# Kernel optimization log

Hardware: AMD Instinct MI355X
Metric: run time of the kernel (lower is better)

Reference implementation:

```python
import jax, jax.numpy as jnp
import numpy as np

K = 20          # neighbors, hardcoded in module
SLOPE = 0.2     # LeakyReLU negative slope
EPS = 1e-5      # BatchNorm eps (eval mode, running_mean=0, running_var=1)


def _knn_idx(x, k):
    # x: (B, N, C) -> (B, N, k) indices of k nearest neighbors (includes self)
    xx = jnp.sum(x * x, axis=-1)                      # (B, N)
    inner = jnp.einsum('bnc,bmc->bnm', x, x)          # (B, N, N)
    neg_sqdist = 2.0 * inner - xx[:, :, None] - xx[:, None, :]
    _, idx = jax.lax.top_k(neg_sqdist, k)
    return idx


def _graph_feature(x, k):
    # x: (B, N, C) -> edge features (B, N, k, 2C) = [x_j - x_i, x_i]
    idx = _knn_idx(x, k)
    feat = jax.vmap(lambda xt, ix: xt[ix])(x, idx)    # (B, N, k, C)
    xc = jnp.broadcast_to(x[:, :, None, :], feat.shape)
    return jnp.concatenate([feat - xc, xc], axis=-1)


def _bn_lrelu(h, g, b):
    # eval-mode BN (mean=0, var=1) + LeakyReLU(0.2)
    h = h * (g / jnp.sqrt(1.0 + EPS)) + b
    return jnp.where(h >= 0, h, SLOPE * h)


def _edge_conv(x, W, g, b):
    # EdgeConv block: graph feature -> 1x1 conv -> BN -> LeakyReLU -> max over k
    e = _graph_feature(x, K)                          # (B, N, k, 2C)
    h = jnp.einsum('bnkc,oc->bnko', e, W)
    h = _bn_lrelu(h, g, b)
    return jnp.max(h, axis=2)                         # (B, N, O)


def reference(x, W1, g1, b1, W2, g2, b2, W3, g3, b3, W4, g4, b4, W5, g5, b5, Wemb):
    # x: (B, N, 3) point cloud
    x1 = _edge_conv(x, W1, g1, b1)    # (B, N, 64)
    x2 = _edge_conv(x1, W2, g2, b2)   # (B, N, 64)
    x3 = _edge_conv(x2, W3, g3, b3)   # (B, N, 128)
    x4 = _edge_conv(x3, W4, g4, b4)   # (B, N, 256)
    h = jnp.concatenate([x1, x2, x3, x4], axis=-1)    # (B, N, 512)
    h = jnp.einsum('bnc,oc->bno', h, W5)              # conv5 (1x1)
    h = _bn_lrelu(h, g5, b5)
    h = jnp.max(h, axis=1)                            # global max pool -> (B, 512)
    feat = h[:, None, :]                              # (B, 1, 512)
    embedding = h @ Wemb.T                            # (B, 256)
    return (feat, embedding)


def setup_inputs() -> dict:
    key = jax.random.key(0)
    ks = jax.random.split(key, 18)
    B, N = 8, 2048
    num_features = 256

    def w(k, o, i):
        return jax.random.normal(k, (o, i), dtype=jnp.float32) * (1.0 / np.sqrt(i))

    return {
        'x':  jax.random.normal(ks[0], (B, N, 3), dtype=jnp.float32),
        'W1': w(ks[1], 64, 6),
        'g1': jnp.ones((64,), jnp.float32),  'b1': jnp.zeros((64,), jnp.float32),
        'W2': w(ks[2], 64, 128),
        'g2': jnp.ones((64,), jnp.float32),  'b2': jnp.zeros((64,), jnp.float32),
        'W3': w(ks[3], 128, 128),
        'g3': jnp.ones((128,), jnp.float32), 'b3': jnp.zeros((128,), jnp.float32),
        'W4': w(ks[4], 256, 256),
        'g4': jnp.ones((256,), jnp.float32), 'b4': jnp.zeros((256,), jnp.float32),
        'W5': w(ks[5], 512, 512),
        'g5': jnp.ones((512,), jnp.float32), 'b5': jnp.zeros((512,), jnp.float32),
        'Wemb': w(ks[6], num_features, 512),
    }
```

## Files before the change

kernel.cpp:

```cpp
#include <hip/hip_runtime.h>
#include <hip/hip_bf16.h>

#define BB 8
#define NN 2048
#define KK 20
#define BN (BB*NN)
#define RSQ 0.99999500003749969f

constexpr size_t OFF_XX  = 0;
constexpr size_t OFF_X1  = OFF_XX  + BN;
constexpr size_t OFF_X2  = OFF_X1  + (size_t)BN*64;
constexpr size_t OFF_X3  = OFF_X2  + (size_t)BN*64;
constexpr size_t OFF_X4  = OFF_X3  + (size_t)BN*128;
constexpr size_t OFF_SC  = OFF_X4  + (size_t)BN*256;
constexpr size_t OFF_ID  = OFF_SC  + (size_t)BN*160;
constexpr size_t OFF_W5T = OFF_ID  + (size_t)BN*20;
constexpr size_t OFF_MX  = OFF_W5T + 512*512;
constexpr size_t OFF_MN  = OFF_MX  + BB*512;
constexpr size_t OFF_WT2 = OFF_MN  + BB*512;
constexpr size_t OFF_WT3 = OFF_WT2 + 8192;
constexpr size_t OFF_WT4 = OFF_WT3 + 16384;
constexpr size_t WS_END  = OFF_WT4 + 65536;
constexpr size_t OFF_BIG = WS_END;
constexpr size_t OFF_XCAT = OFF_BIG + (size_t)16*1024*1024;
constexpr size_t WS_BIG_END = OFF_BIG + (size_t)BB*NN*NN;
static_assert(OFF_ID - OFF_X3 >= (size_t)4096*2048, "fallback dual dist fits");
static_assert(OFF_XCAT + (size_t)BN*768 <= WS_BIG_END, "xcat h/m/l fits in dist region");

typedef unsigned short u16;
typedef __attribute__((ext_vector_type(8))) short short8;
typedef __attribute__((ext_vector_type(8))) unsigned short ushort8;
typedef __attribute__((ext_vector_type(4))) float f32x4;

constexpr size_t WTS_2H = 0,      WTS_2M = 8192,   WTS_2L = 16384;
constexpr size_t WTS_3H = 24576,  WTS_3M = 40960,  WTS_3L = 57344;
constexpr size_t WTS_4H = 73728,  WTS_4M = 139264, WTS_4L = 204800;

__device__ inline unsigned encf(float f){ unsigned u=__float_as_uint(f); return (u&0x80000000u)? ~u : (u|0x80000000u); }
__device__ inline float decf(unsigned e){ unsigned u=(e&0x80000000u)? (e&0x7fffffffu) : ~e; return __uint_as_float(u); }
__device__ inline float lrelu(float h){ return h>=0.f ? h : 0.2f*h; }
__device__ inline u16 bf16rne(float x){
  unsigned u = __float_as_uint(x);
  return (u16)((u + 0x7FFFu + ((u>>16)&1u)) >> 16);
}
__device__ inline float bf16f(u16 h){ return __uint_as_float((unsigned)h<<16); }
__device__ inline void bf16split3(float v, u16& h, u16& m, u16& l){
  h = bf16rne(v);  float r1 = v  - bf16f(h);
  m = bf16rne(r1); float r2 = r1 - bf16f(m);
  l = bf16rne(r2);
}

__device__ inline float readlane_f(float v, int sl){
  return __int_as_float(__builtin_amdgcn_readlane(__float_as_int(v), sl));
}

#define INSERT_CAND(cv, ci) { \
  unsigned long long mge = __ballot((lv > cv) || (lv == cv && li < ci)); \
  int pos = __popcll(mge); \
  float upv = __shfl_up(lv, 1); \
  int   upi = __shfl_up(li, 1); \
  bool shift = (lane > pos) && (lane < KK); \
  lv = (lane == pos) ? cv : (shift ? upv : lv); \
  li = (lane == pos) ? ci : (shift ? upi : li); \
  theta = readlane_f(lv, KK-1); }

#define BITONIC64_DESC(v, vi) { \
  _Pragma("unroll") \
  for(int k=2; k<=64; k<<=1){ \
    _Pragma("unroll") \
    for(int j=k>>1; j>=1; j>>=1){ \
      float ov = __shfl_xor(v, j); \
      int   oi = __shfl_xor(vi, j); \
      int partner = lane ^ j; \
      bool keepFirst = (((lane & k) == 0)) == (lane < partner); \
      bool before = (v > ov) || (v == ov && vi < oi); \
      if(keepFirst != before){ v = ov; vi = oi; } \
    } \
  } }

#define MFMA6(ACC, AH, AM, AL, BH, BM, BL) { \
  ACC = __builtin_amdgcn_mfma_f32_16x16x32_bf16(AH, BH, ACC, 0, 0, 0); \
  ACC = __builtin_amdgcn_mfma_f32_16x16x32_bf16(AH, BM, ACC, 0, 0, 0); \
  ACC = __builtin_amdgcn_mfma_f32_16x16x32_bf16(AM, BH, ACC, 0, 0, 0); \
  ACC = __builtin_amdgcn_mfma_f32_16x16x32_bf16(AH, BL, ACC, 0, 0, 0); \
  ACC = __builtin_amdgcn_mfma_f32_16x16x32_bf16(AL, BH, ACC, 0, 0, 0); \
  ACC = __builtin_amdgcn_mfma_f32_16x16x32_bf16(AM, BM, ACC, 0, 0, 0); }


__global__ void prep_k(const float* W5, const float* W2, const float* W3, const float* W4,
                       float* W5T, float* WT2, float* WT3, float* WT4,
                       u16* w5h, u16* w5m, u16* w5l, u16* wts,
                       unsigned* mx, unsigned* mn, int big){
  int i = blockIdx.x*256 + threadIdx.x;
  if(!big){ int o = i>>9, c = i&511; W5T[c*512+o] = W5[i]; }
  {
    int rg = i>>13, kt = (i>>9)&15, l = (i>>3)&63, j = i&7;
    int o = rg*16 + (l&15);
    int c = kt*32 + ((l>>4)<<3) + j;
    u16 h,m,lo; bf16split3(W5[(size_t)o*512 + c], h, m, lo);
    w5h[i]=h; w5m[i]=m; w5l[i]=lo; }
  if(i < 65536){ int c = i>>9, o = i&511;
    WT4[i] = (o<256) ? W4[(size_t)o*256 + c] : W4[(size_t)(o-256)*256 + 128 + c]; }
  if(i < 16384){ int c = i>>8, o = i&255;
    WT3[i] = (o<128) ? W3[(size_t)o*128 + c] : W3[(size_t)(o-128)*128 + 64 + c]; }
  if(i <  8192){ int c = i>>7, o = i&127;
    WT2[i] = (o<64) ? W2[(size_t)o*128 + c] : W2[(size_t)(o-64)*128 + 64 + c]; }
  if(big){
    if(i < 65536){
      int rg=i>>11, kt=(i>>9)&3, l=(i>>3)&63, j=i&7;
      int o = rg*16 + (l&15);
      int c = kt*32 + ((l>>4)<<3) + j;
      float v = (o<256) ? W4[(size_t)o*256 + c] : W4[(size_t)(o-256)*256 + 128 + c];
      u16 h,m,lo; bf16split3(v,h,m,lo);
      wts[WTS_4H+i]=h; wts[WTS_4M+i]=m; wts[WTS_4L+i]=lo; }
    if(i < 16384){
      int rg=i>>10, kt=(i>>9)&1, l=(i>>3)&63, j=i&7;
      int o = rg*16 + (l&15);
      int c = kt*32 + ((l>>4)<<3) + j;
      float v = (o<128) ? W3[(size_t)o*128 + c] : W3[(size_t)(o-128)*128 + 64 + c];
      u16 h,m,lo; bf16split3(v,h,m,lo);
      wts[WTS_3H+i]=h; wts[WTS_3M+i]=m; wts[WTS_3L+i]=lo; }
    if(i < 8192){
      int rg=i>>10, kt=(i>>9)&1, l=(i>>3)&63, j=i&7;
      int o = rg*16 + (l&15);
      int c = kt*32 + ((l>>4)<<3) + j;
      float v = (o<64) ? W2[(size_t)o*128 + c] : W2[(size_t)(o-64)*128 + 64 + c];
      u16 h,m,lo; bf16split3(v,h,m,lo);
      wts[WTS_2H+i]=h; wts[WTS_2M+i]=m; wts[WTS_2L+i]=lo; }
  }
  if(i <  4096){ mx[i] = 0x007FFFFFu; mn[i] = 0xFF800000u; }
}

template<int C>
__launch_bounds__(256) __global__ void sqnorm_k(const float* X, float* xx){
  int i = blockIdx.x*256 + threadIdx.x;
  const float* r = X + (size_t)i*C;
  float s = 0.f;
  #pragma unroll
  for(int c=0;c<C;c++) s = fmaf(r[c], r[c], s);
  xx[i] = s;
}

template<int C>
__launch_bounds__(256) __global__ void split_k(const float* __restrict__ X,
    u16* __restrict__ xh, u16* __restrict__ xm, u16* __restrict__ xl){
  constexpr int KT = C/32;
  const size_t t = (size_t)blockIdx.x*256 + threadIdx.x;
  const int l = (int)(t & 63);
  const size_t tile = t >> 6;
  const int kt = (int)(tile & (KT-1));
  const size_t rgG = tile / KT;
  const size_t row = rgG*16 + (l & 15);
  const int k = kt*32 + ((l>>4)<<3);
  const float* p = X + row*C + k;
  float4 v0 = *(const float4*)p;
  float4 v1 = *(const float4*)(p+4);
  float vs[8] = {v0.x,v0.y,v0.z,v0.w,v1.x,v1.y,v1.z,v1.w};
  ushort8 H,M,L;
  #pragma unroll
  for(int j=0;j<8;j++){ u16 h,m,lo; bf16split3(vs[j],h,m,lo); H[j]=h; M[j]=m; L[j]=lo; }
  *(ushort8*)(xh + t*8) = H;
  *(ushort8*)(xm + t*8) = M;
  *(ushort8*)(xl + t*8) = L;
}

#define FMA_ROW(I) \
  acc[I][0]=fmaf(a,b0v,acc[I][0]); acc[I][1]=fmaf(a,b1v,acc[I][1]); \
  acc[I][2]=fmaf(a,b2v,acc[I][2]); acc[I][3]=fmaf(a,b3v,acc[I][3]); \
  acc[I][4]=fmaf(a,b4v,acc[I][4]); acc[I][5]=fmaf(a,b5v,acc[I][5]); \
  acc[I][6]=fmaf(a,b6v,acc[I][6]); acc[I][7]=fmaf(a,b7v,acc[I][7]);

template<int C>
__launch_bounds__(256) __global__ void gemm_dist_k(const float* __restrict__ X, const float* __restrict__ xx,
                                                   float* __restrict__ dist, int b0){
  constexpr int AST = 188;
  __shared__ __align__(16) float a_sh[16*AST];
  __shared__ __align__(16) float b_sh[16*AST];
  __shared__ float sxn[128], sxm[128];
  const int tid = threadIdx.x;
  const int b   = b0 + blockIdx.z;
  const int mtile = blockIdx.x*128;
  const int ntile = blockIdx.y*128;
  const int tn = tid & 15, tm = tid >> 4;
  const float* Xb  = X  + (size_t)b*NN*C;
  const float* xxb = xx + (size_t)b*NN;
  if(tid < 128) sxn[tid] = xxb[ntile + tid];
  else          sxm[tid-128] = xxb[mtile + tid-128];
  float acc[8][8];
  #pragma unroll
  for(int i=0;i<8;i++){
    #pragma unroll
    for(int j=0;j<8;j++) acc[i][j]=0.f;
  }
  for(int cc=0; cc<C; cc+=16){
    __syncthreads();
    #pragma unroll
    for(int s=0;s<2;s++){
      int ii = tid + 256*s; int r = ii>>2, q = ii&3;
      int pr = r + 4*(r>>3);
      float4 va = *(const float4*)&Xb[(size_t)(ntile + r)*C + cc + 4*q];
      a_sh[(4*q+0)*AST + pr]=va.x; a_sh[(4*q+1)*AST + pr]=va.y;
      a_sh[(4*q+2)*AST + pr]=va.z; a_sh[(4*q+3)*AST + pr]=va.w;
      float4 vb = *(const float4*)&Xb[(size_t)(mtile + r)*C + cc + 4*q];
      b_sh[(4*q+0)*AST + pr]=vb.x; b_sh[(4*q+1)*AST + pr]=vb.y;
      b_sh[(4*q+2)*AST + pr]=vb.z; b_sh[(4*q+3)*AST + pr]=vb.w;
    }
    __syncthreads();
    #pragma unroll
    for(int c=0;c<16;c++){
      float4 A0 = *(const float4*)&a_sh[c*AST + 12*tn];
      float4 A1 = *(const float4*)&a_sh[c*AST + 12*tn + 4];
      float4 B0 = *(const float4*)&b_sh[c*AST + 12*tm];
      float4 B1 = *(const float4*)&b_sh[c*AST + 12*tm + 4];
      float b0v=B0.x,b1v=B0.y,b2v=B0.z,b3v=B0.w,b4v=B1.x,b5v=B1.y,b6v=B1.z,b7v=B1.w;
      float a;
      a=A0.x; FMA_ROW(0)
      a=A0.y; FMA_ROW(1)
      a=A0.z; FMA_ROW(2)
      a=A0.w; FMA_ROW(3)
      a=A1.x; FMA_ROW(4)
      a=A1.y; FMA_ROW(5)
      a=A1.z; FMA_ROW(6)
      a=A1.w; FMA_ROW(7)
    }
  }
  float xnr[8], xmr[8];
  #pragma unroll
  for(int i=0;i<8;i++){ xnr[i]=sxn[tn*8+i]; xmr[i]=sxm[tm*8+i]; }
  const size_t rowb = (size_t)blockIdx.z*NN + ntile + tn*8;
  #pragma unroll
  for(int i=0;i<8;i++){
    float4 w0, w1;
    w0.x=(2.f*acc[i][0]-xnr[i])-xmr[0]; w0.y=(2.f*acc[i][1]-xnr[i])-xmr[1];
    w0.z=(2.f*acc[i][2]-xnr[i])-xmr[2]; w0.w=(2.f*acc[i][3]-xnr[i])-xmr[3];
    w1.x=(2.f*acc[i][4]-xnr[i])-xmr[4]; w1.y=(2.f*acc[i][5]-xnr[i])-xmr[5];
    w1.z=(2.f*acc[i][6]-xnr[i])-xmr[6]; w1.w=(2.f*acc[i][7]-xnr[i])-xmr[7];
    float* dp = dist + (rowb + i)*NN + mtile + tm*8;
    *(float4*)dp = w0;
    *(float4*)(dp+4) = w1;
  }
}

template<int C>
__launch_bounds__(256) __global__ void mfma_dist_k(const u16* __restrict__ xh, const u16* __restrict__ xm,
    const u16* __restrict__ xl, const float* __restrict__ xx, float* __restrict__ dist, int b0){
  constexpr int KT = C/32;
  const int tid = threadIdx.x;
  const int l  = tid & 63, wv = tid >> 6;
  const int lg = l >> 4, lr = l & 15;
  const int cz = blockIdx.z;
  const int b  = b0 + cz;
  const int qrow0 = blockIdx.y*128 + (wv>>1)*64;
  const int crow0 = blockIdx.x*64 + (wv&1)*32;
  const size_t brg = (size_t)b*(NN/16);
  f32x4 acc[4][2];
  #pragma unroll
  for(int m=0;m<4;m++){
    #pragma unroll
    for(int n=0;n<2;n++) acc[m][n] = (f32x4){0.f,0.f,0.f,0.f};
  }
  const size_t abase = (brg + (qrow0>>4))*KT*512 + (size_t)l*8;
  const size_t bbase = (brg + (crow0>>4))*KT*512 + (size_t)l*8;
  for(int kt=0; kt<KT; kt++){
    short8 Ah[4], Am[4], Al[4], Bh[2], Bm[2], Bl[2];
    #pragma unroll
    for(int m=0;m<4;m++){
      size_t o = abase + (size_t)(m*KT + kt)*512;
      Ah[m] = *(const short8*)(xh + o);
      Am[m] = *(const short8*)(xm + o);
      Al[m] = *(const short8*)(xl + o);
    }
    #pragma unroll
    for(int n=0;n<2;n++){
      size_t o = bbase + (size_t)(n*KT + kt)*512;
      Bh[n] = *(const short8*)(xh + o);
      Bm[n] = *(const short8*)(xm + o);
      Bl[n] = *(const short8*)(xl + o);
    }
    #pragma unroll
    for(int m=0;m<4;m++){
      #pragma unroll
      for(int n=0;n<2;n++){
        MFMA6(acc[m][n], Ah[m], Am[m], Al[m], Bh[n], Bm[n], Bl[n])
      }
    }
  }
  const float* xxb = xx + (size_t)b*NN;
  float xxc[2];
  #pragma unroll
  for(int n=0;n<2;n++) xxc[n] = xxb[crow0 + n*16 + lr];
  #pragma unroll
  for(int m=0;m<4;m++){
    #pragma unroll
    for(int r=0;r<4;r++){
      int qr = qrow0 + m*16 + 4*lg + r;
      float xq = xxb[qr];
      float* dp = dist + ((size_t)cz*NN + qr)*NN + crow0;
      #pragma unroll
      for(int n=0;n<2;n++) dp[n*16 + lr] = (2.f*acc[m][n][r] - xq) - xxc[n];
    }
  }
}

__launch_bounds__(256) __global__ void sel_k(const float* __restrict__ dist, int* __restrict__ id,
                                             int b0, int nrows){
  const int w = (blockIdx.x*256 + threadIdx.x) >> 6;
  const int lane = threadIdx.x & 63;
  if(w >= nrows) return;
  const float* dr = dist + (size_t)w*NN;
  float4 c0 = *(const float4*)&dr[4*lane];
  float cd0[4] = {c0.x, c0.y, c0.z, c0.w};
  int jbest = 0; float v = cd0[0];
  #pragma unroll
  for(int j=1;j<4;j++){ if(cd0[j] > v){ v = cd0[j]; jbest = j; } }
  int vi = 4*lane + jbest;
  BITONIC64_DESC(v, vi)
  float lv = (lane < KK) ? v : -INFINITY;
  int   li = (lane < KK) ? vi : 0;
  float theta = readlane_f(lv, KK-1);
  #pragma unroll
  for(int j=0;j<4;j++){
    float cand = (j == jbest) ? -INFINITY : cd0[j];
    unsigned long long bal = __ballot(cand > theta);
    while(bal){
      int bpos = __ffsll((unsigned long long)bal) - 1;
      bal &= bal - 1;
      float cv = readlane_f(cand, bpos);
      if(cv > theta){
        int ci = 4*bpos + j;
        INSERT_CAND(cv, ci)
      }
    }
  }
  for(int ms=256; ms<NN; ms+=256){
    float4 c4 = *(const float4*)&dr[ms + 4*lane];
    #pragma unroll
    for(int j=0;j<4;j++){
      float cand = (j==0)?c4.x:(j==1)?c4.y:(j==2)?c4.z:c4.w;
      unsigned long long bal = __ballot(cand > theta);
      while(bal){
        int bpos = __ffsll((unsigned long long)bal) - 1;
        bal &= bal - 1;
        float cv = readlane_f(cand, bpos);
        if(cv > theta){
          int ci = ms + 4*bpos + j;
          INSERT_CAND(cv, ci)
        }
      }
    }
  }
  if(lane < KK) id[((size_t)b0*NN + w)*KK + lane] = li;
}

__launch_bounds__(256) __global__ void sel3_k(const float* __restrict__ X, int* __restrict__ id){
  const int gw = (blockIdx.x*256 + threadIdx.x) >> 6;
  const int lane = threadIdx.x & 63;
  const int b = gw >> 11, n = gw & 2047;
  const float* Xb  = X + (size_t)b*NN*3;
  const float x0v = Xb[n*3], x1v = Xb[n*3+1], x2v = Xb[n*3+2];
  float xxn = 0.f;
  xxn = fmaf(x0v, x0v, xxn); xxn = fmaf(x1v, x1v, xxn); xxn = fmaf(x2v, x2v, xxn);
  float lv, theta; int li;
  {
    const float* p = Xb + (size_t)(4*lane)*3;
    float4 va = *(const float4*)p;
    float4 vb = *(const float4*)(p+4);
    float4 vc = *(const float4*)(p+8);
    float cx[4] = {va.x, va.w, vb.z, vc.y};
    float cy[4] = {va.y, vb.x, vb.w, vc.z};
    float cz[4] = {va.z, vb.y, vc.x, vc.w};
    float cd[4];
    #pragma unroll
    for(int j=0;j<4;j++){
      float s = 0.f;
      s = fmaf(x0v, cx[j], s); s = fmaf(x1v, cy[j], s); s = fmaf(x2v, cz[j], s);
      float xxm = 0.f;
      xxm = fmaf(cx[j], cx[j], xxm); xxm = fmaf(cy[j], cy[j], xxm); xxm = fmaf(cz[j], cz[j], xxm);
      cd[j] = (2.f*s - xxn) - xxm;
    }
    int jbest = 0; float v = cd[0];
    #pragma unroll
    for(int j=1;j<4;j++){ if(cd[j] > v){ v = cd[j]; jbest = j; } }
    int vi = 4*lane + jbest;
    BITONIC64_DESC(v, vi)
    lv = (lane < KK) ? v : -INFINITY;
    li = (lane < KK) ? vi : 0;
    theta = readlane_f(lv, KK-1);
    #pragma unroll
    for(int j=0;j<4;j++){
      float cand = (j == jbest) ? -INFINITY : cd[j];
      unsigned long long bal = __ballot(cand > theta);
      while(bal){
        int bpos = __ffsll((unsigned long long)bal) - 1;
        bal &= bal - 1;
        float cv = readlane_f(cand, bpos);
        if(cv > theta){
          int ci = 4*bpos + j;
          INSERT_CAND(cv, ci)
        }
      }
    }
  }
  for(int ms=256; ms<NN; ms+=256){
    const float* p = Xb + (size_t)(ms + 4*lane)*3;
    float4 va = *(const float4*)p;
    float4 vb = *(const float4*)(p+4);
    float4 vc = *(const float4*)(p+8);
    float cx[4] = {va.x, va.w, vb.z, vc.y};
    float cy[4] = {va.y, vb.x, vb.w, vc.z};
    float cz[4] = {va.z, vb.y, vc.x, vc.w};
    float cd[4];
    #pragma unroll
    for(int j=0;j<4;j++){
      float s = 0.f;
      s = fmaf(x0v, cx[j], s); s = fmaf(x1v, cy[j], s); s = fmaf(x2v, cz[j], s);
      float xxm = 0.f;
      xxm = fmaf(cx[j], cx[j], xxm); xxm = fmaf(cy[j], cy[j], xxm); xxm = fmaf(cz[j], cz[j], xxm);
      cd[j] = (2.f*s - xxn) - xxm;
    }
    #pragma unroll
    for(int j=0;j<4;j++){
      float cand = cd[j];
      unsigned long long bal = __ballot(cand > theta);
      while(bal){
        int bpos = __ffsll((unsigned long long)bal) - 1;
        bal &= bal - 1;
        float cv = readlane_f(cand, bpos);
        if(cv > theta){
          int ci = ms + 4*bpos + j;
          INSERT_CAND(cv, ci)
        }
      }
    }
  }
  if(lane < KK) id[(size_t)gw*KK + lane] = li;
}

__launch_bounds__(256) __global__ void qp3_k(const float* X, const float* W, float* qp){
  const int t   = blockIdx.x*256 + threadIdx.x;
  const int row = t >> 3;
  const int c0  = (t & 7) * 8;
  float xn[3];
  #pragma unroll
  for(int c=0;c<3;c++) xn[c] = X[(size_t)row*3 + c];
  for(int oi=c0; oi<c0+8; oi++){
    const float* w = W + (size_t)oi*6;
    float aq=0.f, ap=0.f;
    #pragma unroll
    for(int c=0;c<3;c++){ aq = fmaf(xn[c], w[c], aq); ap = fmaf(xn[c], w[3+c], ap); }
    qp[(size_t)row*128 + oi]      = aq;
    qp[(size_t)row*128 + 64 + oi] = ap;
  }
}

template<int KT, int W2C>
__launch_bounds__(256) __global__ void qp_mfma_k(const u16* __restrict__ xh, const u16* __restrict__ xm,
    const u16* __restrict__ xl,
    const u16* __restrict__ wh, const u16* __restrict__ wm, const u16* __restrict__ wl,
    float* __restrict__ qp){
  const int tid = threadIdx.x;
  const int l  = tid & 63, wv = tid >> 6;
  const int lg = l >> 4, lr = l & 15;
  const int row0 = blockIdx.x*128 + (wv>>1)*64;
  const int col0 = blockIdx.y*64 + (wv&1)*32;
  f32x4 acc[4][2];
  #pragma unroll
  for(int m=0;m<4;m++){
    #pragma unroll
    for(int n=0;n<2;n++) acc[m][n] = (f32x4){0.f,0.f,0.f,0.f};
  }
  const size_t abase = (size_t)(row0>>4)*KT*512 + (size_t)l*8;
  const size_t bbase = (size_t)(col0>>4)*KT*512 + (size_t)l*8;
  for(int kt=0; kt<KT; kt++){
    short8 Ah[4], Am[4], Al[4], Bh[2], Bm[2], Bl[2];
    #pragma unroll
    for(int m=0;m<4;m++){
      size_t o = abase + (size_t)(m*KT + kt)*512;
      Ah[m] = *(const short8*)(xh + o);
      Am[m] = *(const short8*)(xm + o);
      Al[m] = *(const short8*)(xl + o);
    }
    #pragma unroll
    for(int n=0;n<2;n++){
      size_t o = bbase + (size_t)(n*KT + kt)*512;
      Bh[n] = *(const short8*)(wh + o);
      Bm[n] = *(const short8*)(wm + o);
      Bl[n] = *(const short8*)(wl + o);
    }
    #pragma unroll
    for(int m=0;m<4;m++){
      #pragma unroll
      for(int n=0;n<2;n++){
        MFMA6(acc[m][n], Ah[m], Am[m], Al[m], Bh[n], Bm[n], Bl[n])
      }
    }
  }
  #pragma unroll
  for(int m=0;m<4;m++){
    #pragma unroll
    for(int r=0;r<4;r++){
      int row = row0 + m*16 + 4*lg + r;
      float* dp = qp + (size_t)row*W2C + col0;
      #pragma unroll
      for(int n=0;n<2;n++) dp[n*16 + lr] = acc[m][n][r];
    }
  }
}

template<int COUT>
__launch_bounds__(256) __global__ void gather_qp_k(const float* __restrict__ qp, const int* __restrict__ idx,
    const float* g, const float* bb, float* out){
  const int t  = blockIdx.x*256 + threadIdx.x;
  const int o  = t % COUT;
  const int bn = t / COUT;
  const int b  = bn >> 11;
  const int* id = idx + (size_t)bn*KK;
  float qv = qp[(size_t)bn*(2*COUT) + o];
  float pv = qp[(size_t)bn*(2*COUT) + COUT + o];
  float base = pv - qv;
  float mx = -INFINITY, mn = INFINITY;
  #pragma unroll
  for(int k=0;k<KK;k++){
    int ik = id[k];
    float v = qp[((size_t)((b<<11) + ik))*(2*COUT) + o];
    mx = fmaxf(mx, v); mn = fminf(mn, v);
  }
  float a  = g[o] * RSQ;
  float bo = bb[o];
  out[(size_t)bn*COUT + o] = lrelu((a >= 0.f ? a*(mx+base) : a*(mn+base)) + bo);
}

template<int CIN, int COUT>
__launch_bounds__(256) __global__ void qp64T_k(const float* __restrict__ X, const float* __restrict__ WT,
                                               int cb, float* __restrict__ q, float* __restrict__ bs){
  const int t   = blockIdx.x*256 + threadIdx.x;
  const int row = t >> 3;
  const int o0  = cb + (t & 7) * 8;
  float xn[CIN];
  #pragma unroll
  for(int c=0;c<CIN;c+=4){ float4 v = *(const float4*)(X + (size_t)row*CIN + c);
    xn[c]=v.x; xn[c+1]=v.y; xn[c+2]=v.z; xn[c+3]=v.w; }
  float aq[8], ap[8];
  #pragma unroll
  for(int j=0;j<8;j++){ aq[j]=0.f; ap[j]=0.f; }
  #pragma unroll 4
  for(int c=0;c<CIN;c++){
    float xc = xn[c];
    float4 wa0 = *(const float4*)&WT[(size_t)c*(2*COUT) + o0];
    float4 wa1 = *(const float4*)&WT[(size_t)c*(2*COUT) + o0 + 4];
    float4 wb0 = *(const float4*)&WT[(size_t)c*(2*COUT) + COUT + o0];
    float4 wb1 = *(const float4*)&WT[(size_t)c*(2*COUT) + COUT + o0 + 4];
    aq[0]=fmaf(xc,wa0.x,aq[0]); aq[1]=fmaf(xc,wa0.y,aq[1]); aq[2]=fmaf(xc,wa0.z,aq[2]); aq[3]=fmaf(xc,wa0.w,aq[3]);
    aq[4]=fmaf(xc,wa1.x,aq[4]); aq[5]=fmaf(xc,wa1.y,aq[5]); aq[6]=fmaf(xc,wa1.z,aq[6]); aq[7]=fmaf(xc,wa1.w,aq[7]);
    ap[0]=fmaf(xc,wb0.x,ap[0]); ap[1]=fmaf(xc,wb0.y,ap[1]); ap[2]=fmaf(xc,wb0.z,ap[2]); ap[3]=fmaf(xc,wb0.w,ap[3]);
    ap[4]=fmaf(xc,wb1.x,ap[4]); ap[5]=fmaf(xc,wb1.y,ap[5]); ap[6]=fmaf(xc,wb1.z,ap[6]); ap[7]=fmaf(xc,wb1.w,ap[7]);
  }
  float* qpp = q  + (size_t)row*64 + (o0-cb);
  float* bpp = bs + (size_t)row*64 + (o0-cb);
  *(float4*)qpp     = make_float4(aq[0],aq[1],aq[2],aq[3]);
  *(float4*)(qpp+4) = make_float4(aq[4],aq[5],aq[6],aq[7]);
  *(float4*)bpp     = make_float4(ap[0]-aq[0],ap[1]-aq[1],ap[2]-aq[2],ap[3]-aq[3]);
  *(float4*)(bpp+4) = make_float4(ap[4]-aq[4],ap[5]-aq[5],ap[6]-aq[6],ap[7]-aq[7]);
}

template<int CFULL>
__launch_bounds__(256) __global__ void gather_chunk_k(const float* q, const float* bs, const int* idx,
    const float* g, const float* bb, int cb, float* out){
  const int t  = blockIdx.x*256 + threadIdx.x;
  const int o  = t & 63;
  const int bn = t >> 6;
  const int b  = bn >> 11;
  const int* id = idx + (size_t)bn*KK;
  float base = bs[t];
  float mx = -INFINITY, mn = INFINITY;
  #pragma unroll
  for(int k=0;k<KK;k++){
    int ik = id[k];
    float v = q[((size_t)((b<<11) + ik))*64 + o];
    mx = fmaxf(mx, v); mn = fminf(mn, v);
  }
  float a  = g[cb+o] * RSQ;
  float bo = bb[cb+o];
  out[(size_t)bn*CFULL + cb + o] = lrelu((a >= 0.f ? a*(mx+base) : a*(mn+base)) + bo);
}

__launch_bounds__(256) __global__ void w5gemm_k(const float* __restrict__ x1, const float* __restrict__ x2,
    const float* __restrict__ x3, const float* __restrict__ x4,
    const float* __restrict__ W5T, unsigned* mxe, unsigned* mne){
  constexpr int ASTA = 92;
  constexpr int ASTB = 188;
  __shared__ __align__(16) float a_sh[16*ASTA];
  __shared__ __align__(16) float b_sh[16*ASTB];
  const int tid = threadIdx.x;
  const int otile = blockIdx.x*128;
  const int rtile = blockIdx.y*64;
  const int b     = blockIdx.z;
  const int tn = tid & 15, tm = tid >> 4;
  const int aoff = 4*tn + 4*(tn>>1);
  const size_t row0 = (size_t)b*NN + rtile;
  float acc[4][8];
  #pragma unroll
  for(int i=0;i<4;i++){
    #pragma unroll
    for(int j=0;j<8;j++) acc[i][j]=0.f;
  }
  for(int cc=0; cc<512; cc+=16){
    const float* src; int stride, coff;
    if(cc<64)      { src=x1; stride=64;  coff=cc; }
    else if(cc<128){ src=x2; stride=64;  coff=cc-64; }
    else if(cc<256){ src=x3; stride=128; coff=cc-128; }
    else           { src=x4; stride=256; coff=cc-256; }
    __syncthreads();
    { int r = tid>>2, q = tid&3;
      int pr = r + 4*(r>>3);
      float4 va = *(const float4*)&src[(row0 + r)*stride + coff + 4*q];
      a_sh[(4*q+0)*ASTA + pr]=va.x; a_sh[(4*q+1)*ASTA + pr]=va.y;
      a_sh[(4*q+2)*ASTA + pr]=va.z; a_sh[(4*q+3)*ASTA + pr]=va.w; }
    #pragma unroll
    for(int s=0;s<2;s++){
      int ii = tid + 256*s;
      int cl = ii>>5, o4 = ii&31;
      float4 vb = *(const float4*)&W5T[(size_t)(cc+cl)*512 + otile + 4*o4];
      *(float4*)&b_sh[cl*ASTB + 4*o4 + 4*(o4>>1)] = vb;
    }
    __syncthreads();
    #pragma unroll
    for(int c=0;c<16;c++){
      float4 A0 = *(const float4*)&a_sh[c*ASTA + aoff];
      float4 B0 = *(const float4*)&b_sh[c*ASTB + 12*tm];
      float4 B1 = *(const float4*)&b_sh[c*ASTB + 12*tm + 4];
      float b0v=B0.x,b1v=B0.y,b2v=B0.z,b3v=B0.w,b4v=B1.x,b5v=B1.y,b6v=B1.z,b7v=B1.w;
      float a;
      a=A0.x; FMA_ROW(0)
      a=A0.y; FMA_ROW(1)
      a=A0.z; FMA_ROW(2)
      a=A0.w; FMA_ROW(3)
    }
  }
  #pragma unroll
  for(int j=0;j<8;j++){
    float M=-INFINITY, m=INFINITY;
    #pragma unroll
    for(int i=0;i<4;i++){ M=fmaxf(M,acc[i][j]); m=fminf(m,acc[i][j]); }
    #pragma unroll
    for(int d=1; d<16; d<<=1){
      M = fmaxf(M, __shfl_xor(M, d));
      m = fminf(m, __shfl_xor(m, d));
    }
    if(tn == 0){
      int o = otile + tm*8 + j;
      atomicMax(&mxe[b*512+o], encf(M));
      atomicMin(&mne[b*512+o], encf(m));
    }
  }
}

__launch_bounds__(256) __global__ void cvt_k(const float* __restrict__ x1, const float* __restrict__ x2,
    const float* __restrict__ x3, const float* __restrict__ x4,
    u16* __restrict__ xh, u16* __restrict__ xm, u16* __restrict__ xl){
  const size_t t = (size_t)blockIdx.x*256 + threadIdx.x;
  const int l = (int)(t & 63);
  const size_t tile = t >> 6;
  const int kt = (int)(tile & 15);
  const size_t rgG = tile >> 4;
  const size_t row = rgG*16 + (l & 15);
  const int col = kt*32 + ((l>>4)<<3);
  const float* src; int stride, coff;
  if(col<64)      { src=x1; stride=64;  coff=col; }
  else if(col<128){ src=x2; stride=64;  coff=col-64; }
  else if(col<256){ src=x3; stride=128; coff=col-128; }
  else            { src=x4; stride=256; coff=col-256; }
  const float* p = src + row*stride + coff;
  float4 v0 = *(const float4*)p;
  float4 v1 = *(const float4*)(p+4);
  float vs[8] = {v0.x,v0.y,v0.z,v0.w,v1.x,v1.y,v1.z,v1.w};
  ushort8 H, M, L;
  #pragma unroll
  for(int j=0;j<8;j++){ u16 h,m,lo; bf16split3(vs[j],h,m,lo); H[j]=h; M[j]=m; L[j]=lo; }
  *(ushort8*)(xh + t*8) = H;
  *(ushort8*)(xm + t*8) = M;
  *(ushort8*)(xl + t*8) = L;
}

__launch_bounds__(256) __global__ void w5mfma_k(const u16* __restrict__ xh, const u16* __restrict__ xm,
    const u16* __restrict__ xl,
    const u16* __restrict__ wh, const u16* __restrict__ wm, const u16* __restrict__ wl,
    unsigned* mxe, unsigned* mne){
  const int tid = threadIdx.x;
  const int l  = tid & 63, wv = tid >> 6;
  const int lg = l >> 4, lr = l & 15;
  const int row0 = blockIdx.x*128 + (wv>>1)*64;
  const int col0 = blockIdx.y*64 + (wv&1)*32;
  const int b = blockIdx.x >> 4;
  f32x4 acc[4][2];
  #pragma unroll
  for(int m=0;m<4;m++){
    #pragma unroll
    for(int n=0;n<2;n++) acc[m][n] = (f32x4){0.f,0.f,0.f,0.f};
  }
  const size_t abase = (size_t)(row0>>4)*16*512 + (size_t)l*8;
  const size_t bbase = (size_t)(col0>>4)*16*512 + (size_t)l*8;
  for(int kt=0; kt<16; kt++){
    short8 Ah[4], Am[4], Al[4], Bh[2], Bm[2], Bl[2];
    #pragma unroll
    for(int m=0;m<4;m++){
      size_t o = abase + (size_t)(m*16 + kt)*512;
      Ah[m] = *(const short8*)(xh + o);
      Am[m] = *(const short8*)(xm + o);
      Al[m] = *(const short8*)(xl + o);
    }
    #pragma unroll
    for(int n=0;n<2;n++){
      size_t o = bbase + (size_t)(n*16 + kt)*512;
      Bh[n] = *(const short8*)(wh + o);
      Bm[n] = *(const short8*)(wm + o);
      Bl[n] = *(const short8*)(wl + o);
    }
    #pragma unroll
    for(int m=0;m<4;m++){
      #pragma unroll
      for(int n=0;n<2;n++){
        MFMA6(acc[m][n], Ah[m], Am[m], Al[m], Bh[n], Bm[n], Bl[n])
      }
    }
  }
  #pragma unroll
  for(int n=0;n<2;n++){
    float M = -INFINITY, mnv = INFINITY;
    #pragma unroll
    for(int m=0;m<4;m++){
      #pragma unroll
      for(int r=0;r<4;r++){ float v = acc[m][n][r]; M = fmaxf(M, v); mnv = fminf(mnv, v); }
    }
    M   = fmaxf(M,   __shfl_xor(M, 16));   M   = fmaxf(M,   __shfl_xor(M, 32));
    mnv = fminf(mnv, __shfl_xor(mnv, 16)); mnv = fminf(mnv, __shfl_xor(mnv, 32));
    if(lg == 0){
      int o = col0 + n*16 + lr;
      atomicMax(&mxe[b*512+o], encf(M));
      atomicMin(&mne[b*512+o], encf(mnv));
    }
  }
}

__launch_bounds__(256) __global__ void final_k(const unsigned* mxe, const unsigned* mne,
    const float* g5, const float* b5, const float* Wemb, float* out){
  const int b = blockIdx.x, t = threadIdx.x;
  __shared__ float h[512];
  for(int o=t; o<512; o+=256){
    float mx = decf(mxe[b*512+o]);
    float mn = decf(mne[b*512+o]);
    float a  = g5[o] * RSQ;
    float bo = b5[o];
    float hv = lrelu((a >= 0.f ? a*mx : a*mn) + bo);
    h[o] = hv;
    out[b*512+o] = hv;
  }
  __syncthreads();
  const float* wr = Wemb + (size_t)t*512;
  float s = 0.f;
  for(int o=0;o<512;o+=4){
    float4 w4 = *(const float4*)(wr+o);
    s = fmaf(h[o],w4.x, fmaf(h[o+1],w4.y, fmaf(h[o+2],w4.z, fmaf(h[o+3],w4.w, s))));
  }
  out[4096 + b*256 + t] = s;
}

extern "C" void kernel_launch(void* const* d_in, const int* in_sizes, int n_in,
                              void* d_out, int out_size, void* d_ws, size_t ws_size,
                              hipStream_t stream) {
  if (ws_size < WS_END * sizeof(float)) return;
  const bool big = ws_size >= WS_BIG_END * sizeof(float);

  const float* x0   = (const float*)d_in[0];
  const float* W1   = (const float*)d_in[1];
  const float* g1   = (const float*)d_in[2];
  const float* b1   = (const float*)d_in[3];
  const float* W2   = (const float*)d_in[4];
  const float* g2   = (const float*)d_in[5];
  const float* b2   = (const float*)d_in[6];
  const float* W3   = (const float*)d_in[7];
  const float* g3   = (const float*)d_in[8];
  const float* b3   = (const float*)d_in[9];
  const float* W4   = (const float*)d_in[10];
  const float* g4   = (const float*)d_in[11];
  const float* b4   = (const float*)d_in[12];
  const float* W5   = (const float*)d_in[13];
  const float* g5   = (const float*)d_in[14];
  const float* b5   = (const float*)d_in[15];
  const float* Wemb = (const float*)d_in[16];

  float* ws = (float*)d_ws;
  float* xx = ws + OFF_XX;
  float* x1 = ws + OFF_X1;  float* x2 = ws + OFF_X2;
  float* x3 = ws + OFF_X3;  float* x4 = ws + OFF_X4;
  float* qpS = ws + OFF_SC;
  float* bsS = ws + OFF_SC + (size_t)BN*64;
  int*   id = (int*)(ws + OFF_ID);
  float* W5Tf = ws + OFF_W5T;
  unsigned* mxe = (unsigned*)(ws + OFF_MX);
  unsigned* mne = (unsigned*)(ws + OFF_MN);
  float* WT2 = ws + OFF_WT2;
  float* WT3 = ws + OFF_WT3;
  float* WT4 = ws + OFF_WT4;
  float* distD = ws + OFF_X3;
  float* distS = ws + OFF_X4;
  float* distB = ws + OFF_BIG;
  u16* w5h = (u16*)(ws + OFF_SC + (size_t)BN*128);
  u16* w5m = w5h + 512*512;
  u16* w5l = w5m + 512*512;
  u16* wts = (u16*)W5Tf;
  float* out = (float*)d_out;

  prep_k<<<1024,256,0,stream>>>(W5, W2, W3, W4, W5Tf, WT2, WT3, WT4,
                                w5h, w5m, w5l, wts, mxe, mne, big ? 1 : 0);

  sel3_k<<<BN*64/256,256,0,stream>>>(x0, id);
  qp3_k<<<BN*8/256,256,0,stream>>>(x0, W1, qpS);
  gather_qp_k<64><<<BN*64/256,256,0,stream>>>(qpS, id, g1, b1, x1);

  if(big){
    float* qpB = distB;
    u16* sh = (u16*)x4;
    { u16* sm = sh + (size_t)BN*64; u16* sl = sm + (size_t)BN*64;
      sqnorm_k<64><<<BN/256,256,0,stream>>>(x1, xx);
      split_k<64><<<BN*64/8/256,256,0,stream>>>(x1, sh, sm, sl);
      for(int c0=0;c0<BB;c0+=4){
        mfma_dist_k<64><<<dim3(32,16,4),256,0,stream>>>(sh, sm, sl, xx, distB, c0);
        sel_k<<<(4*NN)/4,256,0,stream>>>(distB, id, c0, 4*NN);
      }
      qp_mfma_k<2,128><<<dim3(BN/128,2),256,0,stream>>>(sh, sm, sl,
          wts+WTS_2H, wts+WTS_2M, wts+WTS_2L, qpB);
      gather_qp_k<64><<<BN*64/256,256,0,stream>>>(qpB, id, g2, b2, x2); }
    { u16* sm = sh + (size_t)BN*64; u16* sl = sm + (size_t)BN*64;
      sqnorm_k<64><<<BN/256,256,0,stream>>>(x2, xx);
      split_k<64><<<BN*64/8/256,256,0,stream>>>(x2, sh, sm, sl);
      for(int c0=0;c0<BB;c0+=4){
        mfma_dist_k<64><<<dim3(32,16,4),256,0,stream>>>(sh, sm, sl, xx, distB, c0);
        sel_k<<<(4*NN)/4,256,0,stream>>>(distB, id, c0, 4*NN);
      }
      qp_mfma_k<2,256><<<dim3(BN/128,4),256,0,stream>>>(sh, sm, sl,
          wts+WTS_3H, wts+WTS_3M, wts+WTS_3L, qpB);
      gather_qp_k<128><<<BN*128/256,256,0,stream>>>(qpB, id, g3, b3, x3); }
    { u16* sm = sh + (size_t)BN*128; u16* sl = sm + (size_t)BN*128;
      sqnorm_k<128><<<BN/256,256,0,stream>>>(x3, xx);
      split_k<128><<<BN*128/8/256,256,0,stream>>>(x3, sh, sm, sl);
      for(int c0=0;c0<BB;c0+=4){
        mfma_dist_k<128><<<dim3(32,16,4),256,0,stream>>>(sh, sm, sl, xx, distB, c0);
        sel_k<<<(4*NN)/4,256,0,stream>>>(distB, id, c0, 4*NN);
      }
      qp_mfma_k<4,512><<<dim3(BN/128,8),256,0,stream>>>(sh, sm, sl,
          wts+WTS_4H, wts+WTS_4M, wts+WTS_4L, qpB);
      gather_qp_k<256><<<BN*256/256,256,0,stream>>>(qpB, id, g4, b4, x4); }
    u16* xh = (u16*)(ws + OFF_XCAT);
    u16* xm = xh + (size_t)BN*512;
    u16* xl = xm + (size_t)BN*512;
    cvt_k<<<BN*512/8/256,256,0,stream>>>(x1, x2, x3, x4, xh, xm, xl);
    w5mfma_k<<<dim3(128,8),256,0,stream>>>(xh, xm, xl, w5h, w5m, w5l, mxe, mne);
  } else {
    sqnorm_k<64><<<BN/256,256,0,stream>>>(x1, xx);
    for(int r=0;r<4;r++){
      gemm_dist_k<64><<<dim3(16,16,2),256,0,stream>>>(x1, xx, distD, 2*r);
      sel_k<<<(2*NN)/4,256,0,stream>>>(distD, id, 2*r, 2*NN);
    }
    qp64T_k<64,64><<<BN*8/256,256,0,stream>>>(x1, WT2, 0, qpS, bsS);
    gather_chunk_k<64><<<BN*64/256,256,0,stream>>>(qpS, bsS, id, g2, b2, 0, x2);

    sqnorm_k<64><<<BN/256,256,0,stream>>>(x2, xx);
    for(int r=0;r<4;r++){
      gemm_dist_k<64><<<dim3(16,16,2),256,0,stream>>>(x2, xx, distD, 2*r);
      sel_k<<<(2*NN)/4,256,0,stream>>>(distD, id, 2*r, 2*NN);
    }
    for(int cb=0; cb<128; cb+=64){
      qp64T_k<64,128><<<BN*8/256,256,0,stream>>>(x2, WT3, cb, qpS, bsS);
      gather_chunk_k<128><<<BN*64/256,256,0,stream>>>(qpS, bsS, id, g3, b3, cb, x3);
    }

    sqnorm_k<128><<<BN/256,256,0,stream>>>(x3, xx);
    for(int r=0;r<8;r++){
      gemm_dist_k<128><<<dim3(16,16,1),256,0,stream>>>(x3, xx, distS, r);
      sel_k<<<NN/4,256,0,stream>>>(distS, id, r, NN);
    }
    for(int cb=0; cb<256; cb+=64){
      qp64T_k<128,256><<<BN*8/256,256,0,stream>>>(x3, WT4, cb, qpS, bsS);
      gather_chunk_k<256><<<BN*64/256,256,0,stream>>>(qpS, bsS, id, g4, b4, cb, x4);
    }
    w5gemm_k<<<dim3(4,32,8),256,0,stream>>>(x1, x2, x3, x4, W5Tf, mxe, mne);
  }

  final_k<<<BB,256,0,stream>>>(mxe, mne, g5, b5, Wemb, out);
}
```

Before: 603.4 us.

## Stage MFMA operand tiles through LDS in distance and conv5 kernels

Both the pairwise-distance MFMA kernel and the conv5 MFMA kernel now cooperatively load each k-step's A and B fragments (hi/mid/lo bf16 splits) into shared memory, then every wave reads its fragments from LDS. Before, each wave loaded its own fragments straight from global memory, so fragments shared between waves were fetched twice. This cuts duplicated global traffic but adds two barriers per k-step and gives no double buffering, so load latency is no longer hidden by the register prefetch.

New measurement: 634.2 us. 5.1% more time.

```diff
diff --git a/kernel.cpp b/kernel.cpp
--- a/kernel.cpp
+++ b/kernel.cpp
@@ -245,6 +245,7 @@
 __launch_bounds__(256) __global__ void mfma_dist_k(const u16* __restrict__ xh, const u16* __restrict__ xm,
     const u16* __restrict__ xl, const float* __restrict__ xx, float* __restrict__ dist, int b0){
   constexpr int KT = C/32;
+  __shared__ u16 lds[36*512];
   const int tid = threadIdx.x;
   const int l  = tid & 63, wv = tid >> 6;
   const int lg = l >> 4, lr = l & 15;
@@ -253,35 +254,46 @@
   const int qrow0 = blockIdx.y*128 + (wv>>1)*64;
   const int crow0 = blockIdx.x*64 + (wv&1)*32;
   const size_t brg = (size_t)b*(NN/16);
+  const size_t rgA = brg + (size_t)blockIdx.y*8;
+  const size_t rgB = brg + (size_t)blockIdx.x*4;
   f32x4 acc[4][2];
   #pragma unroll
   for(int m=0;m<4;m++){
     #pragma unroll
     for(int n=0;n<2;n++) acc[m][n] = (f32x4){0.f,0.f,0.f,0.f};
   }
-  const size_t abase = (brg + (qrow0>>4))*KT*512 + (size_t)l*8;
-  const size_t bbase = (brg + (crow0>>4))*KT*512 + (size_t)l*8;
   for(int kt=0; kt<KT; kt++){
-    short8 Ah[4], Am[4], Al[4], Bh[2], Bm[2], Bl[2];
-    #pragma unroll
-    for(int m=0;m<4;m++){
-      size_t o = abase + (size_t)(m*KT + kt)*512;
-      Ah[m] = *(const short8*)(xh + o);
-      Am[m] = *(const short8*)(xm + o);
-      Al[m] = *(const short8*)(xl + o);
-    }
-    #pragma unroll
-    for(int n=0;n<2;n++){
-      size_t o = bbase + (size_t)(n*KT + kt)*512;
-      Bh[n] = *(const short8*)(xh + o);
-      Bm[n] = *(const short8*)(xm + o);
-      Bl[n] = *(const short8*)(xl + o);
-    }
-    #pragma unroll
-    for(int m=0;m<4;m++){
+    __syncthreads();
+    #pragma unroll
+    for(int p=0;p<9;p++){
+      int c  = p*4 + (tid>>6);
+      int ln = tid & 63;
+      const u16* src; size_t off;
+      if(c < 24){ int s = c>>3, rg = c&7;
+        src = (s==0) ? xh : (s==1) ? xm : xl;
+        off = ((rgA + rg)*KT + kt)*512 + (size_t)ln*8;
+      } else { int cc = c-24; int s = cc>>2, cg = cc&3;
+        src = (s==0) ? xh : (s==1) ? xm : xl;
+        off = ((rgB + cg)*KT + kt)*512 + (size_t)ln*8;
+      }
+      *(ushort8*)&lds[c*512 + ln*8] = *(const ushort8*)(src + off);
+    }
+    __syncthreads();
+    short8 Bh[2], Bm[2], Bl[2];
+    #pragma unroll
+    for(int n=0;n<2;n++){ int cg = (wv&1)*2 + n;
+      Bh[n] = *(const short8*)&lds[(24+cg)*512 + l*8];
+      Bm[n] = *(const short8*)&lds[(28+cg)*512 + l*8];
+      Bl[n] = *(const short8*)&lds[(32+cg)*512 + l*8];
+    }
+    #pragma unroll
+    for(int m=0;m<4;m++){ int rg = (wv>>1)*4 + m;
+      short8 Ah_ = *(const short8*)&lds[(   rg)*512 + l*8];
+      short8 Am_ = *(const short8*)&lds[( 8+rg)*512 + l*8];
+      short8 Al_ = *(const short8*)&lds[(16+rg)*512 + l*8];
       #pragma unroll
       for(int n=0;n<2;n++){
-        MFMA6(acc[m][n], Ah[m], Am[m], Al[m], Bh[n], Bm[n], Bl[n])
+        MFMA6(acc[m][n], Ah_, Am_, Al_, Bh[n], Bm[n], Bl[n])
       }
     }
   }
@@ -686,41 +698,52 @@
     const u16* __restrict__ xl,
     const u16* __restrict__ wh, const u16* __restrict__ wm, const u16* __restrict__ wl,
     unsigned* mxe, unsigned* mne){
+  __shared__ u16 lds[36*512];
   const int tid = threadIdx.x;
   const int l  = tid & 63, wv = tid >> 6;
   const int lg = l >> 4, lr = l & 15;
-  const int row0 = blockIdx.x*128 + (wv>>1)*64;
   const int col0 = blockIdx.y*64 + (wv&1)*32;
   const int b = blockIdx.x >> 4;
+  const size_t rgA = (size_t)blockIdx.x*8;
+  const size_t cgB = (size_t)blockIdx.y*4;
   f32x4 acc[4][2];
   #pragma unroll
   for(int m=0;m<4;m++){
     #pragma unroll
     for(int n=0;n<2;n++) acc[m][n] = (f32x4){0.f,0.f,0.f,0.f};
   }
-  const size_t abase = (size_t)(row0>>4)*16*512 + (size_t)l*8;
-  const size_t bbase = (size_t)(col0>>4)*16*512 + (size_t)l*8;
   for(int kt=0; kt<16; kt++){
-    short8 Ah[4], Am[4], Al[4], Bh[2], Bm[2], Bl[2];
-    #pragma unroll
-    for(int m=0;m<4;m++){
-      size_t o = abase + (size_t)(m*16 + kt)*512;
-      Ah[m] = *(const short8*)(xh + o);
-      Am[m] = *(const short8*)(xm + o);
-      Al[m] = *(const short8*)(xl + o);
-    }
-    #pragma unroll
-    for(int n=0;n<2;n++){
-      size_t o = bbase + (size_t)(n*16 + kt)*512;
-      Bh[n] = *(const short8*)(wh + o);
-      Bm[n] = *(const short8*)(wm + o);
-      Bl[n] = *(const short8*)(wl + o);
-    }
-    #pragma unroll
-    for(int m=0;m<4;m++){
+    __syncthreads();
+    #pragma unroll
+    for(int p=0;p<9;p++){
+      int c  = p*4 + (tid>>6);
+      int ln = tid & 63;
+      const u16* src; size_t off;
+      if(c < 24){ int s = c>>3, rg = c&7;
+        src = (s==0) ? xh : (s==1) ? xm : xl;
+        off = ((rgA + rg)*16 + kt)*512 + (size_t)ln*8;
+      } else { int cc = c-24; int s = cc>>2, cg = cc&3;
+        src = (s==0) ? wh : (s==1) ? wm : wl;
+        off = ((cgB + cg)*16 + kt)*512 + (size_t)ln*8;
+      }
+      *(ushort8*)&lds[c*512 + ln*8] = *(const ushort8*)(src + off);
+    }
+    __syncthreads();
+    short8 Bh[2], Bm[2], Bl[2];
+    #pragma unroll
+    for(int n=0;n<2;n++){ int cg = (wv&1)*2 + n;
+      Bh[n] = *(const short8*)&lds[(24+cg)*512 + l*8];
+      Bm[n] = *(const short8*)&lds[(28+cg)*512 + l*8];
+      Bl[n] = *(const short8*)&lds[(32+cg)*512 + l*8];
+    }
+    #pragma unroll
+    for(int m=0;m<4;m++){ int rg = (wv>>1)*4 + m;
+      short8 Ah_ = *(const short8*)&lds[(   rg)*512 + l*8];
+      short8 Am_ = *(const short8*)&lds[( 8+rg)*512 + l*8];
+      short8 Al_ = *(const short8*)&lds[(16+rg)*512 + l*8];
       #pragma unroll
       for(int n=0;n<2;n++){
-        MFMA6(acc[m][n], Ah[m], Am[m], Al[m], Bh[n], Bm[n], Bl[n])
+        MFMA6(acc[m][n], Ah_, Am_, Al_, Bh[n], Bm[n], Bl[n])
       }
     }
   }
```
